# Performance work log

Measured on AMD Instinct MI355X. Metric: run time of the kernel, lower is better.

Reference implementation:

```python
import jax, jax.numpy as jnp
import numpy as np

DIM = 512
HEADS = 8
DIM_HEAD = 64
NUM_MEM_KV = 4
H = W = 128


def setup_inputs() -> dict:
    key = jax.random.key(0)
    k1, k2, k3, k4 = jax.random.split(key, 4)
    return {
        "x": jax.random.normal(k1, (DIM, H, W), dtype=jnp.float32),
        "norm1_gamma": jnp.zeros((DIM, 1, 1), dtype=jnp.float32),
        "qkv_w": jax.random.normal(k2, (3 * HEADS * DIM_HEAD, DIM), dtype=jnp.float32) * (DIM ** -0.5),
        "mem_kv": jax.random.normal(k3, (2, HEADS, DIM_HEAD, NUM_MEM_KV), dtype=jnp.float32),
        "conv_w": jax.random.normal(k4, (DIM, HEADS * DIM_HEAD), dtype=jnp.float32) * ((HEADS * DIM_HEAD) ** -0.5),
        "conv_b": jnp.zeros((DIM,), dtype=jnp.float32),
        "norm2_gamma": jnp.zeros((DIM, 1, 1), dtype=jnp.float32),
    }


def rms_norm(x, gamma, dim):
    # x: (c, h, w); L2 norm over channel axis, rescale by sqrt(dim)*(gamma+1)
    n = jnp.linalg.norm(x, ord=2, axis=0)  # (h, w)
    return x / n * (gamma + 1.0) * (dim ** 0.5)


def reference(x, norm1_gamma, qkv_w, mem_kv, conv_w, conv_b, norm2_gamma):
    c, h, w = x.shape
    scale = DIM_HEAD ** -0.5
    xn = rms_norm(x, norm1_gamma, DIM)
    # 1x1 conv == channel matmul
    qkv = jnp.einsum('oc,cxy->oxy', qkv_w, xn)  # (3*hidden, h, w)
    q, k, v = jnp.split(qkv, 3, axis=0)
    def to_heads(t):
        return t.reshape(HEADS, DIM_HEAD, h * w)  # (H, d, n)
    q, k, v = to_heads(q), to_heads(k), to_heads(v)
    mk, mv = mem_kv[0], mem_kv[1]  # (H, d, m)
    k = jnp.concatenate([mk, k], axis=-1)
    v = jnp.concatenate([mv, v], axis=-1)
    q = jax.nn.softmax(q, axis=-2) * scale  # softmax over feature dim d
    k = jax.nn.softmax(k, axis=-1)          # softmax over sequence dim n
    context = jnp.einsum('hdn,hen->hde', k, v)  # (H, d, e)
    out = jnp.einsum('hde,hdn->hen', context, q)  # (H, e, n)
    out = out.reshape(HEADS * DIM_HEAD, h, w)
    out = jnp.einsum('oc,cxy->oxy', conv_w, out) + conv_b[:, None, None]
    return rms_norm(out, norm2_gamma, DIM)
```

## Files before the change

### kernel.cpp

```cpp
#include <hip/hip_runtime.h>
#include <hip/hip_bf16.h>
#include <cstdint>


typedef unsigned short u16;
typedef unsigned int   u32;
typedef short bf16x8 __attribute__((ext_vector_type(8)));
typedef float f32x4  __attribute__((ext_vector_type(4)));

#define HW    16384
#define CDIM  512
#define SQRTD 22.627416997969522f

#define WAITV8 asm volatile("s_waitcnt vmcnt(8)" ::: "memory")
#define WAITV0 asm volatile("s_waitcnt vmcnt(0)" ::: "memory")
#define WAITL0 asm volatile("s_waitcnt lgkmcnt(0)" ::: "memory")

__device__ __forceinline__ float bflo2f(u32 u) { union {u32 u_; float f;} c; c.u_ = u << 16;        return c.f; }
__device__ __forceinline__ float bfhi2f(u32 u) { union {u32 u_; float f;} c; c.u_ = u & 0xffff0000u; return c.f; }
__device__ __forceinline__ u16 f2bf(float f) {
  u32 x = __builtin_bit_cast(u32, f);
  u32 r = x + 0x7fffu + ((x >> 16) & 1u);
  return (u16)(r >> 16);
}

__device__ __forceinline__ void gload16(const void* g, void* l) {
  __builtin_amdgcn_global_load_lds(
      (const __attribute__((address_space(1))) void*)(uintptr_t)g,
      (__attribute__((address_space(3))) void*)(u32)(uintptr_t)l,
      16, 0, 0);
}

__global__ __launch_bounds__(512) void k_pre(const float* __restrict__ x, const float* __restrict__ g1,
                                             const float* __restrict__ qkvw, const float* __restrict__ memkv,
                                             u16* __restrict__ xnt, u16* __restrict__ wbf,
                                             float* __restrict__ den, float* __restrict__ ctx) {
  __shared__ float tl[512 * 68];
  __shared__ float ssp[8][64];
  __shared__ float rs[64];
  __shared__ float gl[512];
  int t = threadIdx.x, l = t & 63, w = t >> 6;
  int b = blockIdx.x;
  int p0 = b * 64;
  #pragma unroll
  for (int i = 0; i < 16; i++) {
    int idx = i * 512 + t;
    int c = idx >> 4, p4 = (idx & 15) * 4;
    float4 v = *(const float4*)(x + (size_t)c * HW + p0 + p4);
    *(float4*)&tl[c * 68 + p4] = v;
  }
  if (t < 512) gl[t] = 1.0f + g1[t];
  __syncthreads();
  {
    float s = 0.f;
    #pragma unroll
    for (int c = 0; c < 64; c++) {
      float v = tl[(w * 64 + c) * 68 + l];
      s += v * v;
    }
    ssp[w][l] = s;
  }
  __syncthreads();
  if (t < 64) {
    float s = 0.f;
    #pragma unroll
    for (int j = 0; j < 8; j++) s += ssp[j][t];
    rs[t] = SQRTD * rsqrtf(s);
  }
  __syncthreads();
  #pragma unroll
  for (int i = 0; i < 8; i++) {
    int c0 = (i * 8 + w) * 8;
    float sp = rs[l];
    u32 pk[4];
    #pragma unroll
    for (int j = 0; j < 4; j++) {
      float a = tl[(c0 + 2 * j) * 68 + l] * sp * gl[c0 + 2 * j];
      float bq = tl[(c0 + 2 * j + 1) * 68 + l] * sp * gl[c0 + 2 * j + 1];
      pk[j] = (u32)f2bf(a) | ((u32)f2bf(bq) << 16);
    }
    *(uint4*)&xnt[(size_t)(p0 + l) * CDIM + c0] = make_uint4(pk[0], pk[1], pk[2], pk[3]);
  }
  #pragma unroll
  for (int sweep = 0; sweep < 2; sweep++) {
    int idx = (sweep * 256 * 512 + b * 512 + t) * 4;
    if (idx < 1536 * 512) {
      float4 v = *(const float4*)(qkvw + idx);
      ushort4 o; o.x = f2bf(v.x); o.y = f2bf(v.y); o.z = f2bf(v.z); o.w = f2bf(v.w);
      *(ushort4*)(wbf + idx) = o;
    }
  }
  if (b == 0) {
    if (t < 512) {
      int h = t >> 6, d = t & 63;
      const float* mk = memkv + ((size_t)h * 64 + d) * 4;
      den[t] = __expf(mk[0]) + __expf(mk[1]) + __expf(mk[2]) + __expf(mk[3]);
    }
    #pragma unroll
    for (int i = 0; i < 8; i++) {
      int idx = i * 512 + t;
      int hh = idx >> 9;
      (void)hh;
    }
    for (int i = 0; i < 64; i++) {
      int idx = i * 512 + t;
      int h = idx >> 12, de = idx & 4095;
      int d = de >> 6, e = de & 63;
      const float* mk = memkv + ((size_t)h * 64 + d) * 4;
      const float* mv = memkv + (size_t)(512 + h * 64 + e) * 4;
      ctx[idx] = __expf(mk[0]) * mv[0] + __expf(mk[1]) * mv[1]
               + __expf(mk[2]) * mv[2] + __expf(mk[3]) * mv[3];
    }
  }
}

__global__ __launch_bounds__(256, 2) void k_gemm1(const u16* __restrict__ A, const u16* __restrict__ Bt,
                                                  u16* __restrict__ Cb, u16* __restrict__ qT,
                                                  float* __restrict__ den) {
  const int K = CDIM, N = HW;
  __shared__ u16 As[2][128 * 64], Bs[2][128 * 64];
  int t = threadIdx.x;
  int lane = t & 63, w = t >> 6;
  int lq = lane >> 4, lr = lane & 15;
  int wg = blockIdx.x;
  int gt = (wg & 7) * 192 + (wg >> 3);
  int bn = gt / 12, bm = gt % 12;
  int wm = (w >> 1) * 64, wn = (w & 1) * 64;
  f32x4 acc[4][4] = {};
  const u16* Abase = A + (size_t)bm * 128 * K;
  const u16* Bbase = Bt + (size_t)bn * 128 * K;

  auto STAGE = [&](int buf, int kt) {
    #pragma unroll
    for (int i = 0; i < 4; i++) {
      int s = i * 256 + t;
      int row = s >> 3, slot = (s & 7) ^ (row & 7);
      gload16(Abase + (size_t)row * K + kt * 64 + slot * 8, &As[buf][(i * 256 + (w << 6)) * 8]);
    }
    #pragma unroll
    for (int i = 0; i < 4; i++) {
      int s = i * 256 + t;
      int row = s >> 3, slot = (s & 7) ^ (row & 7);
      gload16(Bbase + (size_t)row * K + kt * 64 + slot * 8, &Bs[buf][(i * 256 + (w << 6)) * 8]);
    }
  };
  auto FRAGS = [&](int buf, int kk, bf16x8* af, bf16x8* bv) {
    #pragma unroll
    for (int mi = 0; mi < 4; mi++) {
      int row = wm + mi * 16 + lr;
      int slot = ((kk << 2) + lq) ^ (row & 7);
      af[mi] = *(const bf16x8*)&As[buf][row * 64 + slot * 8];
    }
    #pragma unroll
    for (int nj = 0; nj < 4; nj++) {
      int row = wn + nj * 16 + lr;
      int slot = ((kk << 2) + lq) ^ (row & 7);
      bv[nj] = *(const bf16x8*)&Bs[buf][row * 64 + slot * 8];
    }
  };

  STAGE(0, 0);
  STAGE(1, 1);
  for (int kt = 0; kt < 7; kt++) {
    int buf = kt & 1;
    WAITV8;
    __builtin_amdgcn_s_barrier();
    bf16x8 af0[4], bv0[4], af1[4], bv1[4];
    FRAGS(buf, 0, af0, bv0);
    FRAGS(buf, 1, af1, bv1);
    WAITL0;
    __builtin_amdgcn_s_barrier();
    if (kt < 6) STAGE(buf, kt + 2);
    __builtin_amdgcn_s_setprio(1);
    #pragma unroll
    for (int mi = 0; mi < 4; mi++)
      #pragma unroll
      for (int nj = 0; nj < 4; nj++)
        acc[mi][nj] = __builtin_amdgcn_mfma_f32_16x16x32_bf16(af0[mi], bv0[nj], acc[mi][nj], 0, 0, 0);
    #pragma unroll
    for (int mi = 0; mi < 4; mi++)
      #pragma unroll
      for (int nj = 0; nj < 4; nj++)
        acc[mi][nj] = __builtin_amdgcn_mfma_f32_16x16x32_bf16(af1[mi], bv1[nj], acc[mi][nj], 0, 0, 0);
    __builtin_amdgcn_s_setprio(0);
  }
  {
    WAITV0;
    __builtin_amdgcn_s_barrier();
    bf16x8 af0[4], bv0[4], af1[4], bv1[4];
    FRAGS(1, 0, af0, bv0);
    FRAGS(1, 1, af1, bv1);
    __builtin_amdgcn_s_setprio(1);
    #pragma unroll
    for (int mi = 0; mi < 4; mi++)
      #pragma unroll
      for (int nj = 0; nj < 4; nj++)
        acc[mi][nj] = __builtin_amdgcn_mfma_f32_16x16x32_bf16(af0[mi], bv0[nj], acc[mi][nj], 0, 0, 0);
    #pragma unroll
    for (int mi = 0; mi < 4; mi++)
      #pragma unroll
      for (int nj = 0; nj < 4; nj++)
        acc[mi][nj] = __builtin_amdgcn_mfma_f32_16x16x32_bf16(af1[mi], bv1[nj], acc[mi][nj], 0, 0, 0);
    __builtin_amdgcn_s_setprio(0);
  }

  int cm0 = bm * 128 + wm, cn0 = bn * 128 + wn;
  if (bm < 4) {
    #pragma unroll
    for (int nj = 0; nj < 4; nj++) {
      float e[4][4];
      float s = 0.f;
      #pragma unroll
      for (int mi = 0; mi < 4; mi++)
        #pragma unroll
        for (int r = 0; r < 4; r++) { e[mi][r] = __expf(acc[mi][nj][r]); s += e[mi][r]; }
      s += __shfl_xor(s, 16);
      s += __shfl_xor(s, 32);
      float inv = 1.0f / s;
      int col = cn0 + nj * 16 + lr;
      #pragma unroll
      for (int mi = 0; mi < 4; mi++) {
        ushort4 o;
        o.x = f2bf(e[mi][0] * inv); o.y = f2bf(e[mi][1] * inv);
        o.z = f2bf(e[mi][2] * inv); o.w = f2bf(e[mi][3] * inv);
        *(ushort4*)&qT[(size_t)col * CDIM + cm0 + mi * 16 + lq * 4] = o;
      }
    }
  } else if (bm < 8) {
    #pragma unroll
    for (int mi = 0; mi < 4; mi++)
      #pragma unroll
      for (int r = 0; r < 4; r++) {
        int rowg = cm0 + mi * 16 + lq * 4 + r;
        float rsum = 0.f;
        #pragma unroll
        for (int nj = 0; nj < 4; nj++) {
          float e = __expf(acc[mi][nj][r]);
          rsum += e;
          Cb[(size_t)rowg * N + cn0 + nj * 16 + lr] = f2bf(e);
        }
        rsum += __shfl_xor(rsum, 1); rsum += __shfl_xor(rsum, 2);
        rsum += __shfl_xor(rsum, 4); rsum += __shfl_xor(rsum, 8);
        if (lr == 0) atomicAdd(&den[rowg - 512], rsum);
      }
  } else {
    #pragma unroll
    for (int mi = 0; mi < 4; mi++)
      #pragma unroll
      for (int nj = 0; nj < 4; nj++) {
        int col = cn0 + nj * 16 + lr;
        #pragma unroll
        for (int r = 0; r < 4; r++) {
          int rowg = cm0 + mi * 16 + lq * 4 + r;
          Cb[(size_t)rowg * N + col] = f2bf(acc[mi][nj][r]);
        }
      }
  }
}

__global__ __launch_bounds__(256) void k_ctx(const u16* __restrict__ qkv, float* __restrict__ ctx) {
  __shared__ u16 Ws[64 * 64], Vs[64 * 64];
  int t = threadIdx.x; int lane = t & 63, w = t >> 6, lq = lane >> 4, lr = lane & 15;
  int h = blockIdx.y; int c0 = blockIdx.x * 512;
  const u16* kbase = qkv + (size_t)(512 + h * 64) * HW + c0;
  const u16* vbase = qkv + (size_t)(1024 + h * 64) * HW + c0;
  f32x4 acc[4] = {};
  for (int kt = 0; kt < 8; kt++) {
    #pragma unroll
    for (int i = 0; i < 2; i++) {
      int s = i * 256 + t; int row = s >> 3, sl = (s & 7) ^ (row & 7);
      gload16(kbase + (size_t)row * HW + kt * 64 + sl * 8, &Ws[(i * 256 + (w << 6)) * 8]);
      gload16(vbase + (size_t)row * HW + kt * 64 + sl * 8, &Vs[(i * 256 + (w << 6)) * 8]);
    }
    __syncthreads();
    #pragma unroll
    for (int kk = 0; kk < 2; kk++) {
      int rowa = w * 16 + lr;
      int sla = ((kk << 2) + lq) ^ (rowa & 7);
      bf16x8 af = *(const bf16x8*)&Ws[rowa * 64 + sla * 8];
      #pragma unroll
      for (int nj = 0; nj < 4; nj++) {
        int rowb = nj * 16 + lr;
        int slb = ((kk << 2) + lq) ^ (rowb & 7);
        bf16x8 bv = *(const bf16x8*)&Vs[rowb * 64 + slb * 8];
        acc[nj] = __builtin_amdgcn_mfma_f32_16x16x32_bf16(af, bv, acc[nj], 0, 0, 0);
      }
    }
    __syncthreads();
  }
  #pragma unroll
  for (int nj = 0; nj < 4; nj++)
    #pragma unroll
    for (int r = 0; r < 4; r++) {
      int d = w * 16 + lq * 4 + r, e = nj * 16 + lr;
      atomicAdd(&ctx[(size_t)h * 4096 + d * 64 + e], acc[nj][r]);
    }
}

__global__ __launch_bounds__(256) void k_fold(const float* __restrict__ convw, const float* __restrict__ ctx,
                                              const float* __restrict__ den, u16* __restrict__ Mbf) {
  __shared__ float cn[64 * 65];
  __shared__ float dn[64];
  int t = threadIdx.x;
  int h = blockIdx.x & 7, oc = blockIdx.x >> 3;
  if (t < 64) dn[t] = 0.125f / den[h * 64 + t];
  __syncthreads();
  #pragma unroll
  for (int i = 0; i < 16; i++) {
    int idx = i * 256 + t;
    int d = idx >> 6, e = idx & 63;
    cn[d * 65 + e] = ctx[(size_t)h * 4096 + idx] * dn[d];
  }
  __syncthreads();
  int o = oc * 64 + (t >> 2);
  int d0 = (t & 3) * 16;
  float Wr[64];
  const float* wp = convw + (size_t)o * CDIM + h * 64;
  #pragma unroll
  for (int e4 = 0; e4 < 16; e4++) {
    float4 v = *(const float4*)(wp + e4 * 4);
    Wr[e4 * 4] = v.x; Wr[e4 * 4 + 1] = v.y; Wr[e4 * 4 + 2] = v.z; Wr[e4 * 4 + 3] = v.w;
  }
  float outv[16];
  #pragma unroll
  for (int dd = 0; dd < 16; dd++) {
    float a = 0.f;
    #pragma unroll
    for (int e = 0; e < 64; e++) a += Wr[e] * cn[(d0 + dd) * 65 + e];
    outv[dd] = a;
  }
  #pragma unroll
  for (int j = 0; j < 8; j++) {
    u32 v = (u32)f2bf(outv[j * 2]) | ((u32)f2bf(outv[j * 2 + 1]) << 16);
    *(u32*)&Mbf[(size_t)o * CDIM + h * 64 + d0 + j * 2] = v;
  }
}

__global__ __launch_bounds__(512) void k_gemm2(const u16* __restrict__ A, const u16* __restrict__ Bt,
                                               const float* __restrict__ bias, const float* __restrict__ g2,
                                               float* __restrict__ out) {
  __shared__ u16 As[512 * 64];
  __shared__ u16 Bs[32 * 64];
  __shared__ float css[32];
  int t = threadIdx.x; int lane = t & 63, w = t >> 6, lq = lane >> 4, lr = lane & 15;
  int bn = blockIdx.x;
  if (t < 32) css[t] = 0.f;
  const u16* Bbase = Bt + (size_t)bn * 32 * CDIM;
  f32x4 acc[4][2] = {};
  for (int kt = 0; kt < 8; kt++) {
    #pragma unroll
    for (int i = 0; i < 8; i++) {
      int s = i * 512 + t;
      int row = s >> 3, slot = (s & 7) ^ (row & 7);
      gload16(A + (size_t)row * CDIM + kt * 64 + slot * 8, &As[(i * 512 + (w << 6)) * 8]);
    }
    if (w < 4) {
      int s = t;
      int row = s >> 3, slot = (s & 7) ^ (row & 7);
      gload16(Bbase + (size_t)row * CDIM + kt * 64 + slot * 8, &Bs[(w << 6) * 8]);
    }
    __syncthreads();
    #pragma unroll
    for (int kk = 0; kk < 2; kk++) {
      bf16x8 af[4], bv[2];
      #pragma unroll
      for (int mi = 0; mi < 4; mi++) {
        int row = w * 64 + mi * 16 + lr;
        int slot = ((kk << 2) + lq) ^ (row & 7);
        af[mi] = *(const bf16x8*)&As[row * 64 + slot * 8];
      }
      #pragma unroll
      for (int nj = 0; nj < 2; nj++) {
        int row = nj * 16 + lr;
        int slot = ((kk << 2) + lq) ^ (row & 7);
        bv[nj] = *(const bf16x8*)&Bs[row * 64 + slot * 8];
      }
      __builtin_amdgcn_s_setprio(1);
      #pragma unroll
      for (int mi = 0; mi < 4; mi++)
        #pragma unroll
        for (int nj = 0; nj < 2; nj++)
          acc[mi][nj] = __builtin_amdgcn_mfma_f32_16x16x32_bf16(af[mi], bv[nj], acc[mi][nj], 0, 0, 0);
      __builtin_amdgcn_s_setprio(0);
    }
    __syncthreads();
  }
  float bb[4][4];
  float ps[2] = {0.f, 0.f};
  #pragma unroll
  for (int mi = 0; mi < 4; mi++)
    #pragma unroll
    for (int r = 0; r < 4; r++) {
      int rowg = w * 64 + mi * 16 + lq * 4 + r;
      bb[mi][r] = bias[rowg];
      #pragma unroll
      for (int nj = 0; nj < 2; nj++) {
        float v = acc[mi][nj][r] + bb[mi][r];
        ps[nj] += v * v;
      }
    }
  #pragma unroll
  for (int nj = 0; nj < 2; nj++) {
    ps[nj] += __shfl_xor(ps[nj], 16);
    ps[nj] += __shfl_xor(ps[nj], 32);
  }
  if (lq == 0) {
    atomicAdd(&css[lr], ps[0]);
    atomicAdd(&css[16 + lr], ps[1]);
  }
  __syncthreads();
  float sc[2];
  sc[0] = SQRTD * rsqrtf(css[lr]);
  sc[1] = SQRTD * rsqrtf(css[16 + lr]);
  #pragma unroll
  for (int mi = 0; mi < 4; mi++)
    #pragma unroll
    for (int r = 0; r < 4; r++) {
      int rowg = w * 64 + mi * 16 + lq * 4 + r;
      float g = 1.0f + g2[rowg];
      #pragma unroll
      for (int nj = 0; nj < 2; nj++) {
        float v = acc[mi][nj][r] + bb[mi][r];
        out[(size_t)rowg * HW + bn * 32 + nj * 16 + lr] = v * sc[nj] * g;
      }
    }
}

extern "C" void kernel_launch(void* const* d_in, const int* in_sizes, int n_in,
                              void* d_out, int out_size, void* d_ws, size_t ws_size,
                              hipStream_t stream) {
  (void)in_sizes; (void)n_in; (void)out_size; (void)ws_size;
  const float* x     = (const float*)d_in[0];
  const float* g1    = (const float*)d_in[1];
  const float* qkvw  = (const float*)d_in[2];
  const float* memkv = (const float*)d_in[3];
  const float* convw = (const float*)d_in[4];
  const float* convb = (const float*)d_in[5];
  const float* g2    = (const float*)d_in[6];
  float* out = (float*)d_out;
  char* ws = (char*)d_ws;

  float* den = (float*)(ws);
  float* ctx = (float*)(ws + 4096);
  u16* Mbf   = (u16*)(ws + 139264);
  u16* wbf   = (u16*)(ws + 663552);
  u16* xnt   = (u16*)(ws + 2236416);
  u16* qkv   = (u16*)(ws + 19013632);
  u16* qT    = qkv;

  k_pre<<<256, 512, 0, stream>>>(x, g1, qkvw, memkv, xnt, wbf, den, ctx);
  k_gemm1<<<1536, 256, 0, stream>>>(wbf, xnt, qkv, qT, den);
  k_ctx<<<dim3(32, 8), 256, 0, stream>>>(qkv, ctx);
  k_fold<<<64, 256, 0, stream>>>(convw, ctx, den, Mbf);
  k_gemm2<<<512, 512, 0, stream>>>(Mbf, qT, convb, g2, out);
}
```

Measured before the change: 102.4 us.

## Fuse K/V context reduction into QKV GEMM epilogue and widen gemm2 tiles

Result: slower. 108.1 us (+5.5%).

```diff
diff --git a/kernel.cpp b/kernel.cpp
--- a/kernel.cpp
+++ b/kernel.cpp
@@ -16,8 +16,6 @@
 #define WAITV0 asm volatile("s_waitcnt vmcnt(0)" ::: "memory")
 #define WAITL0 asm volatile("s_waitcnt lgkmcnt(0)" ::: "memory")
 
-__device__ __forceinline__ float bflo2f(u32 u) { union {u32 u_; float f;} c; c.u_ = u << 16;        return c.f; }
-__device__ __forceinline__ float bfhi2f(u32 u) { union {u32 u_; float f;} c; c.u_ = u & 0xffff0000u; return c.f; }
 __device__ __forceinline__ u16 f2bf(float f) {
   u32 x = __builtin_bit_cast(u32, f);
   u32 r = x + 0x7fffu + ((x >> 16) & 1u);
@@ -96,12 +94,6 @@
       const float* mk = memkv + ((size_t)h * 64 + d) * 4;
       den[t] = __expf(mk[0]) + __expf(mk[1]) + __expf(mk[2]) + __expf(mk[3]);
     }
-    #pragma unroll
-    for (int i = 0; i < 8; i++) {
-      int idx = i * 512 + t;
-      int hh = idx >> 9;
-      (void)hh;
-    }
     for (int i = 0; i < 64; i++) {
       int idx = i * 512 + t;
       int h = idx >> 12, de = idx & 4095;
@@ -115,9 +107,9 @@
 }
 
 __global__ __launch_bounds__(256, 2) void k_gemm1(const u16* __restrict__ A, const u16* __restrict__ Bt,
-                                                  u16* __restrict__ Cb, u16* __restrict__ qT,
-                                                  float* __restrict__ den) {
-  const int K = CDIM, N = HW;
+                                                  u16* __restrict__ qT, float* __restrict__ den,
+                                                  float* __restrict__ ctx) {
+  const int K = CDIM;
   __shared__ u16 As[2][128 * 64], Bs[2][128 * 64];
   int t = threadIdx.x;
   int lane = t & 63, w = t >> 6;
@@ -126,8 +118,10 @@
   int gt = (wg & 7) * 192 + (wg >> 3);
   int bn = gt / 12, bm = gt % 12;
   int wm = (w >> 1) * 64, wn = (w & 1) * 64;
+  int h = bm - 4;
+  int rb01 = (bm < 4) ? bm * 128 : 512 + h * 64;
+  int rb23 = (bm < 4) ? bm * 128 : 960 + h * 64;
   f32x4 acc[4][4] = {};
-  const u16* Abase = A + (size_t)bm * 128 * K;
   const u16* Bbase = Bt + (size_t)bn * 128 * K;
 
   auto STAGE = [&](int buf, int kt) {
@@ -135,7 +129,8 @@
     for (int i = 0; i < 4; i++) {
       int s = i * 256 + t;
       int row = s >> 3, slot = (s & 7) ^ (row & 7);
-      gload16(Abase + (size_t)row * K + kt * 64 + slot * 8, &As[buf][(i * 256 + (w << 6)) * 8]);
+      int rb = (i < 2) ? rb01 : rb23;
+      gload16(A + (size_t)(rb + row) * K + kt * 64 + slot * 8, &As[buf][(i * 256 + (w << 6)) * 8]);
     }
     #pragma unroll
     for (int i = 0; i < 4; i++) {
@@ -204,8 +199,8 @@
     __builtin_amdgcn_s_setprio(0);
   }
 
-  int cm0 = bm * 128 + wm, cn0 = bn * 128 + wn;
   if (bm < 4) {
+    int cm0 = bm * 128 + wm, cn0 = bn * 128 + wn;
     #pragma unroll
     for (int nj = 0; nj < 4; nj++) {
       float e[4][4];
@@ -226,75 +221,63 @@
         *(ushort4*)&qT[(size_t)col * CDIM + cm0 + mi * 16 + lq * 4] = o;
       }
     }
-  } else if (bm < 8) {
-    #pragma unroll
-    for (int mi = 0; mi < 4; mi++)
-      #pragma unroll
-      for (int r = 0; r < 4; r++) {
-        int rowg = cm0 + mi * 16 + lq * 4 + r;
-        float rsum = 0.f;
-        #pragma unroll
-        for (int nj = 0; nj < 4; nj++) {
-          float e = __expf(acc[mi][nj][r]);
-          rsum += e;
-          Cb[(size_t)rowg * N + cn0 + nj * 16 + lr] = f2bf(e);
-        }
-        rsum += __shfl_xor(rsum, 1); rsum += __shfl_xor(rsum, 2);
-        rsum += __shfl_xor(rsum, 4); rsum += __shfl_xor(rsum, 8);
-        if (lr == 0) atomicAdd(&den[rowg - 512], rsum);
-      }
   } else {
-    #pragma unroll
-    for (int mi = 0; mi < 4; mi++)
-      #pragma unroll
-      for (int nj = 0; nj < 4; nj++) {
-        int col = cn0 + nj * 16 + lr;
+    __syncthreads();
+    u16* Ks = &As[0][0];
+    u16* Vs = &Bs[0][0];
+    if (w < 2) {
+      #pragma unroll
+      for (int mi = 0; mi < 4; mi++)
         #pragma unroll
         for (int r = 0; r < 4; r++) {
-          int rowg = cm0 + mi * 16 + lq * 4 + r;
-          Cb[(size_t)rowg * N + col] = f2bf(acc[mi][nj][r]);
+          int d = mi * 16 + lq * 4 + r;
+          float rsum = 0.f;
+          #pragma unroll
+          for (int nj = 0; nj < 4; nj++) {
+            float e = __expf(acc[mi][nj][r]);
+            rsum += e;
+            int px = wn + nj * 16 + lr;
+            Ks[d * 128 + (((px >> 3) ^ (d & 7)) << 3) + (px & 7)] = f2bf(e);
+          }
+          rsum += __shfl_xor(rsum, 1); rsum += __shfl_xor(rsum, 2);
+          rsum += __shfl_xor(rsum, 4); rsum += __shfl_xor(rsum, 8);
+          if (lr == 0) atomicAdd(&den[h * 64 + d], rsum);
         }
-      }
-  }
-}
-
-__global__ __launch_bounds__(256) void k_ctx(const u16* __restrict__ qkv, float* __restrict__ ctx) {
-  __shared__ u16 Ws[64 * 64], Vs[64 * 64];
-  int t = threadIdx.x; int lane = t & 63, w = t >> 6, lq = lane >> 4, lr = lane & 15;
-  int h = blockIdx.y; int c0 = blockIdx.x * 512;
-  const u16* kbase = qkv + (size_t)(512 + h * 64) * HW + c0;
-  const u16* vbase = qkv + (size_t)(1024 + h * 64) * HW + c0;
-  f32x4 acc[4] = {};
-  for (int kt = 0; kt < 8; kt++) {
-    #pragma unroll
-    for (int i = 0; i < 2; i++) {
-      int s = i * 256 + t; int row = s >> 3, sl = (s & 7) ^ (row & 7);
-      gload16(kbase + (size_t)row * HW + kt * 64 + sl * 8, &Ws[(i * 256 + (w << 6)) * 8]);
-      gload16(vbase + (size_t)row * HW + kt * 64 + sl * 8, &Vs[(i * 256 + (w << 6)) * 8]);
+    } else {
+      #pragma unroll
+      for (int mi = 0; mi < 4; mi++)
+        #pragma unroll
+        for (int r = 0; r < 4; r++) {
+          int e = mi * 16 + lq * 4 + r;
+          #pragma unroll
+          for (int nj = 0; nj < 4; nj++) {
+            int px = wn + nj * 16 + lr;
+            Vs[e * 128 + (((px >> 3) ^ (e & 7)) << 3) + (px & 7)] = f2bf(acc[mi][nj][r]);
+          }
+        }
     }
     __syncthreads();
-    #pragma unroll
-    for (int kk = 0; kk < 2; kk++) {
-      int rowa = w * 16 + lr;
-      int sla = ((kk << 2) + lq) ^ (rowa & 7);
-      bf16x8 af = *(const bf16x8*)&Ws[rowa * 64 + sla * 8];
+    f32x4 c2[4] = {};
+    #pragma unroll
+    for (int ks = 0; ks < 4; ks++) {
+      int ra = w * 16 + lr;
+      bf16x8 a = *(const bf16x8*)&Ks[ra * 128 + (((ks * 4 + lq) ^ (ra & 7)) << 3)];
       #pragma unroll
       for (int nj = 0; nj < 4; nj++) {
-        int rowb = nj * 16 + lr;
-        int slb = ((kk << 2) + lq) ^ (rowb & 7);
-        bf16x8 bv = *(const bf16x8*)&Vs[rowb * 64 + slb * 8];
-        acc[nj] = __builtin_amdgcn_mfma_f32_16x16x32_bf16(af, bv, acc[nj], 0, 0, 0);
-      }
-    }
-    __syncthreads();
-  }
-  #pragma unroll
-  for (int nj = 0; nj < 4; nj++)
-    #pragma unroll
-    for (int r = 0; r < 4; r++) {
-      int d = w * 16 + lq * 4 + r, e = nj * 16 + lr;
-      atomicAdd(&ctx[(size_t)h * 4096 + d * 64 + e], acc[nj][r]);
-    }
+        int rb2 = nj * 16 + lr;
+        bf16x8 b = *(const bf16x8*)&Vs[rb2 * 128 + (((ks * 4 + lq) ^ (rb2 & 7)) << 3)];
+        c2[nj] = __builtin_amdgcn_mfma_f32_16x16x32_bf16(a, b, c2[nj], 0, 0, 0);
+      }
+    }
+    float* cp = ctx + (size_t)h * 4096;
+    #pragma unroll
+    for (int nj = 0; nj < 4; nj++)
+      #pragma unroll
+      for (int r = 0; r < 4; r++) {
+        int d = w * 16 + lq * 4 + r, e = nj * 16 + lr;
+        atomicAdd(&cp[d * 64 + e], c2[nj][r]);
+      }
+  }
 }
 
 __global__ __launch_bounds__(256) void k_fold(const float* __restrict__ convw, const float* __restrict__ ctx,
@@ -340,13 +323,13 @@
                                                const float* __restrict__ bias, const float* __restrict__ g2,
                                                float* __restrict__ out) {
   __shared__ u16 As[512 * 64];
-  __shared__ u16 Bs[32 * 64];
-  __shared__ float css[32];
+  __shared__ u16 Bs[64 * 64];
+  __shared__ float css[64];
   int t = threadIdx.x; int lane = t & 63, w = t >> 6, lq = lane >> 4, lr = lane & 15;
   int bn = blockIdx.x;
-  if (t < 32) css[t] = 0.f;
-  const u16* Bbase = Bt + (size_t)bn * 32 * CDIM;
-  f32x4 acc[4][2] = {};
+  if (t < 64) css[t] = 0.f;
+  const u16* Bbase = Bt + (size_t)bn * 64 * CDIM;
+  f32x4 acc[4][4] = {};
   for (int kt = 0; kt < 8; kt++) {
     #pragma unroll
     for (int i = 0; i < 8; i++) {
@@ -354,15 +337,14 @@
       int row = s >> 3, slot = (s & 7) ^ (row & 7);
       gload16(A + (size_t)row * CDIM + kt * 64 + slot * 8, &As[(i * 512 + (w << 6)) * 8]);
     }
-    if (w < 4) {
-      int s = t;
-      int row = s >> 3, slot = (s & 7) ^ (row & 7);
+    {
+      int row = t >> 3, slot = (t & 7) ^ (row & 7);
       gload16(Bbase + (size_t)row * CDIM + kt * 64 + slot * 8, &Bs[(w << 6) * 8]);
     }
     __syncthreads();
     #pragma unroll
     for (int kk = 0; kk < 2; kk++) {
-      bf16x8 af[4], bv[2];
+      bf16x8 af[4], bv[4];
       #pragma unroll
       for (int mi = 0; mi < 4; mi++) {
         int row = w * 64 + mi * 16 + lr;
@@ -370,7 +352,7 @@
         af[mi] = *(const bf16x8*)&As[row * 64 + slot * 8];
       }
       #pragma unroll
-      for (int nj = 0; nj < 2; nj++) {
+      for (int nj = 0; nj < 4; nj++) {
         int row = nj * 16 + lr;
         int slot = ((kk << 2) + lq) ^ (row & 7);
         bv[nj] = *(const bf16x8*)&Bs[row * 64 + slot * 8];
@@ -379,14 +361,14 @@
       #pragma unroll
       for (int mi = 0; mi < 4; mi++)
         #pragma unroll
-        for (int nj = 0; nj < 2; nj++)
+        for (int nj = 0; nj < 4; nj++)
           acc[mi][nj] = __builtin_amdgcn_mfma_f32_16x16x32_bf16(af[mi], bv[nj], acc[mi][nj], 0, 0, 0);
       __builtin_amdgcn_s_setprio(0);
     }
     __syncthreads();
   }
   float bb[4][4];
-  float ps[2] = {0.f, 0.f};
+  float ps[4] = {0.f, 0.f, 0.f, 0.f};
   #pragma unroll
   for (int mi = 0; mi < 4; mi++)
     #pragma unroll
@@ -394,24 +376,24 @@
       int rowg = w * 64 + mi * 16 + lq * 4 + r;
       bb[mi][r] = bias[rowg];
       #pragma unroll
-      for (int nj = 0; nj < 2; nj++) {
+      for (int nj = 0; nj < 4; nj++) {
         float v = acc[mi][nj][r] + bb[mi][r];
         ps[nj] += v * v;
       }
     }
   #pragma unroll
-  for (int nj = 0; nj < 2; nj++) {
+  for (int nj = 0; nj < 4; nj++) {
     ps[nj] += __shfl_xor(ps[nj], 16);
     ps[nj] += __shfl_xor(ps[nj], 32);
   }
   if (lq == 0) {
-    atomicAdd(&css[lr], ps[0]);
-    atomicAdd(&css[16 + lr], ps[1]);
-  }
-  __syncthreads();
-  float sc[2];
-  sc[0] = SQRTD * rsqrtf(css[lr]);
-  sc[1] = SQRTD * rsqrtf(css[16 + lr]);
+    #pragma unroll
+    for (int nj = 0; nj < 4; nj++) atomicAdd(&css[nj * 16 + lr], ps[nj]);
+  }
+  __syncthreads();
+  float sc[4];
+  #pragma unroll
+  for (int nj = 0; nj < 4; nj++) sc[nj] = SQRTD * rsqrtf(css[nj * 16 + lr]);
   #pragma unroll
   for (int mi = 0; mi < 4; mi++)
     #pragma unroll
@@ -419,9 +401,9 @@
       int rowg = w * 64 + mi * 16 + lq * 4 + r;
       float g = 1.0f + g2[rowg];
       #pragma unroll
-      for (int nj = 0; nj < 2; nj++) {
+      for (int nj = 0; nj < 4; nj++) {
         float v = acc[mi][nj][r] + bb[mi][r];
-        out[(size_t)rowg * HW + bn * 32 + nj * 16 + lr] = v * sc[nj] * g;
+        out[(size_t)rowg * HW + bn * 64 + nj * 16 + lr] = v * sc[nj] * g;
       }
     }
 }
@@ -445,12 +427,10 @@
   u16* Mbf   = (u16*)(ws + 139264);
   u16* wbf   = (u16*)(ws + 663552);
   u16* xnt   = (u16*)(ws + 2236416);
-  u16* qkv   = (u16*)(ws + 19013632);
-  u16* qT    = qkv;
+  u16* qT    = (u16*)(ws + 19013632);
 
   k_pre<<<256, 512, 0, stream>>>(x, g1, qkvw, memkv, xnt, wbf, den, ctx);
-  k_gemm1<<<1536, 256, 0, stream>>>(wbf, xnt, qkv, qT, den);
-  k_ctx<<<dim3(32, 8), 256, 0, stream>>>(qkv, ctx);
+  k_gemm1<<<1536, 256, 0, stream>>>(wbf, xnt, qT, den, ctx);
   k_fold<<<64, 256, 0, stream>>>(convw, ctx, den, Mbf);
-  k_gemm2<<<512, 512, 0, stream>>>(Mbf, qT, convb, g2, out);
-}
+  k_gemm2<<<256, 512, 0, stream>>>(Mbf, qT, convb, g2, out);
+}
```
